# Kernel optimization log

Hardware: AMD Instinct MI355X
Metric: run time of the kernel (lower is better)

## Reference

```python
import jax, jax.numpy as jnp
import numpy as np

PAST = 12
FUTURE = 12


def setup_inputs() -> dict:
    key = jax.random.key(0)
    k1, k2, k3, k4, k5 = jax.random.split(key, 5)
    B, L, D = 64, 256, 512
    inp = jax.random.normal(k1, (B, L, D), dtype=jnp.float32)
    W_t = jax.random.normal(k2, (FUTURE, PAST), dtype=jnp.float32) / np.sqrt(PAST)
    b_t = jax.random.normal(k3, (FUTURE,), dtype=jnp.float32) * 0.01
    W_s = jax.random.normal(k4, (D, D), dtype=jnp.float32) / np.sqrt(D)
    b_s = jax.random.normal(k5, (D,), dtype=jnp.float32) * 0.01
    return {"inp": inp, "W_t": W_t, "b_t": b_t, "W_s": W_s, "b_s": b_s}


def reference(inp, W_t, b_t, W_s, b_s):
    # inp: [B, L, D]. Sliding windows of size PAST -> W = L - PAST windows.
    B, L, D = inp.shape
    W = L - PAST
    # gather windows: [B, W, PAST, D]
    idx = jnp.arange(W)[:, None] + jnp.arange(PAST)[None, :]  # [W, PAST]
    x_win = inp[:, idx, :]  # [B, W, PAST, D]
    # temporal Linear(PAST -> FUTURE) along window-time axis
    t = jnp.einsum('bwpd,fp->bwfd', x_win, W_t) + b_t[None, None, :, None]
    # spatial Linear(D -> D) along last axis
    out = jnp.einsum('bwfd,ed->bwfe', t, W_s) + b_s
    return out  # [B, W, FUTURE, D]
```

## Files before the change

kernel.cpp:

```cpp
#include <hip/hip_runtime.h>

#define PAST 12
#define FUTURE 12
#define NB 64
#define NL 256
#define ND 512
#define NW 244

typedef unsigned short ushort_t;
typedef __attribute__((ext_vector_type(8))) short short8;
typedef __attribute__((ext_vector_type(4))) float floatx4;

__device__ inline unsigned int f2bf(float x) {
    unsigned int u = __float_as_uint(x);
    return (u + 0x7fffu + ((u >> 16) & 1u)) >> 16;
}

__global__ __launch_bounds__(256) void convert_inp(
    const float* __restrict__ in, ushort_t* __restrict__ out)
{
    const int i = (blockIdx.x * 256 + threadIdx.x) * 8;
    const float4 v0 = *(const float4*)(in + i);
    const float4 v1 = *(const float4*)(in + i + 4);
    uint4 o;
    o.x = f2bf(v0.x) | (f2bf(v0.y) << 16);
    o.y = f2bf(v0.z) | (f2bf(v0.w) << 16);
    o.z = f2bf(v1.x) | (f2bf(v1.y) << 16);
    o.w = f2bf(v1.z) | (f2bf(v1.w) << 16);
    *(uint4*)(out + i) = o;
}

__global__ __launch_bounds__(256) void prep_ws(
    const float* __restrict__ Ws, ushort_t* __restrict__ Wsb, float* __restrict__ S)
{
    const int row = blockIdx.x;
    const int t = threadIdx.x;
    const float2 v = *(const float2*)(Ws + (size_t)row * ND + t * 2);
    *(unsigned int*)(Wsb + (size_t)row * ND + t * 2) = f2bf(v.x) | (f2bf(v.y) << 16);
    float s = v.x + v.y;
#pragma unroll
    for (int o = 32; o > 0; o >>= 1) s += __shfl_down(s, o);
    __shared__ float red[4];
    if ((t & 63) == 0) red[t >> 6] = s;
    __syncthreads();
    if (t == 0) S[row] = red[0] + red[1] + red[2] + red[3];
}

#define BM 128
#define BN 128
#define BK 32

__global__ __launch_bounds__(256) void gemm_spatial(
    const ushort_t* __restrict__ A,
    const ushort_t* __restrict__ Bm,
    ushort_t* __restrict__ Y)
{
    __shared__ ushort_t As[BM * BK];
    __shared__ ushort_t Bs[BN * BK];

    const int tid  = threadIdx.x;
    const int wave = tid >> 6;
    const int lane = tid & 63;
    const int m0 = blockIdx.y * BM;
    const int n0 = blockIdx.x * BN;
    const int wm = (wave >> 1) * 64;
    const int wn = (wave & 1) * 64;

    floatx4 acc[4][4] = {};

    const int row_a = tid >> 2;
    const int ch_a  = (tid & 3) * 8;

    for (int k0 = 0; k0 < ND; k0 += BK) {
        __syncthreads();
#pragma unroll
        for (int r = 0; r < 2; ++r) {
            const ushort_t* ga = A + (size_t)(m0 + row_a + r * 64) * ND + k0 + ch_a;
            __builtin_amdgcn_global_load_lds(
                (const __attribute__((address_space(1))) unsigned int*)ga,
                (__attribute__((address_space(3))) unsigned int*)(As + (r * 256 + wave * 64) * 8),
                16, 0, 0);
        }
#pragma unroll
        for (int r = 0; r < 2; ++r) {
            const ushort_t* gb = Bm + (size_t)(n0 + row_a + r * 64) * ND + k0 + ch_a;
            __builtin_amdgcn_global_load_lds(
                (const __attribute__((address_space(1))) unsigned int*)gb,
                (__attribute__((address_space(3))) unsigned int*)(Bs + (r * 256 + wave * 64) * 8),
                16, 0, 0);
        }
        __syncthreads();

        const ushort_t* a_base = As + (wm + (lane & 15)) * BK + (lane >> 4) * 8;
        const ushort_t* b_base = Bs + (wn + (lane & 15)) * BK + (lane >> 4) * 8;
        short8 a[4], b[4];
#pragma unroll
        for (int t = 0; t < 4; ++t) {
            a[t] = *(const short8*)(a_base + t * 16 * BK);
            b[t] = *(const short8*)(b_base + t * 16 * BK);
        }
#pragma unroll
        for (int i = 0; i < 4; ++i)
#pragma unroll
            for (int j = 0; j < 4; ++j)
                acc[i][j] = __builtin_amdgcn_mfma_f32_16x16x32_bf16(a[i], b[j], acc[i][j], 0, 0, 0);
    }

#pragma unroll
    for (int i = 0; i < 4; ++i) {
        const int m_base = m0 + wm + i * 16 + (lane >> 4) * 4;
#pragma unroll
        for (int j = 0; j < 4; ++j) {
            const int n = n0 + wn + j * 16 + (lane & 15);
#pragma unroll
            for (int r = 0; r < 4; ++r) {
                Y[(size_t)(m_base + r) * ND + n] = (ushort_t)f2bf(acc[i][j][r]);
            }
        }
    }
}

#define WTILE 8

__global__ __launch_bounds__(256) void temporal_kernel(
    const ushort_t* __restrict__ Y,
    const float*    __restrict__ Wt,
    const float*    __restrict__ bt,
    const float*    __restrict__ bs,
    const float*    __restrict__ S,
    float*          __restrict__ Out)
{
    const int tid = threadIdx.x;
    const int b  = blockIdx.y;
    const int w0 = blockIdx.x * WTILE + (tid >> 7) * 4;
    const int eq = (tid & 127) * 4;

    const float4 Sv  = *(const float4*)(S + eq);
    const float4 bsv = *(const float4*)(bs + eq);

    float win[PAST + 3][4];
    const ushort_t* ybase = Y + ((size_t)(b * NL + w0)) * ND + eq;
#pragma unroll
    for (int i = 0; i < PAST + 3; ++i) {
        if (w0 + i < NL) {
            const uint2 v = *(const uint2*)(ybase + (size_t)i * ND);
            win[i][0] = __uint_as_float(v.x << 16);
            win[i][1] = __uint_as_float(v.x & 0xffff0000u);
            win[i][2] = __uint_as_float(v.y << 16);
            win[i][3] = __uint_as_float(v.y & 0xffff0000u);
        } else {
            win[i][0] = win[i][1] = win[i][2] = win[i][3] = 0.f;
        }
    }

#pragma unroll
    for (int w = 0; w < 4; ++w) {
        if (w0 + w < NW) {
            float* orow = Out + ((size_t)(b * NW + (w0 + w)) * FUTURE) * ND + eq;
#pragma unroll
            for (int f = 0; f < FUTURE; ++f) {
                const float btf = bt[f];
                float a0 = fmaf(btf, Sv.x, bsv.x);
                float a1 = fmaf(btf, Sv.y, bsv.y);
                float a2 = fmaf(btf, Sv.z, bsv.z);
                float a3 = fmaf(btf, Sv.w, bsv.w);
#pragma unroll
                for (int p = 0; p < PAST; ++p) {
                    const float c = Wt[f * PAST + p];
                    a0 = fmaf(c, win[w + p][0], a0);
                    a1 = fmaf(c, win[w + p][1], a1);
                    a2 = fmaf(c, win[w + p][2], a2);
                    a3 = fmaf(c, win[w + p][3], a3);
                }
                *(float4*)(orow + (size_t)f * ND) = make_float4(a0, a1, a2, a3);
            }
        }
    }
}

extern "C" void kernel_launch(void* const* d_in, const int* in_sizes, int n_in,
                              void* d_out, int out_size, void* d_ws, size_t ws_size,
                              hipStream_t stream) {
    const float* inp = (const float*)d_in[0];
    const float* Wt  = (const float*)d_in[1];
    const float* bt  = (const float*)d_in[2];
    const float* Ws  = (const float*)d_in[3];
    const float* bs  = (const float*)d_in[4];
    float* out = (float*)d_out;

    const size_t n_inp = (size_t)NB * NL * ND;
    ushort_t* Y     = (ushort_t*)d_ws;
    ushort_t* inp_b = (ushort_t*)((char*)d_ws + n_inp * 2);
    ushort_t* Ws_b  = (ushort_t*)((char*)d_ws + n_inp * 4);
    float*    S     = (float*)((char*)d_ws + n_inp * 4 + (size_t)ND * ND * 2);

    convert_inp<<<dim3(n_inp / 8 / 256), dim3(256), 0, stream>>>(inp, inp_b);
    prep_ws<<<dim3(ND), dim3(256), 0, stream>>>(Ws, Ws_b, S);
    gemm_spatial<<<dim3(ND / BN, (NB * NL) / BM), dim3(256), 0, stream>>>(inp_b, Ws_b, Y);
    temporal_kernel<<<dim3((NW + WTILE - 1) / WTILE, NB), dim3(256), 0, stream>>>(Y, Wt, bt, bs, S, out);
}
```

Baseline: 427.2 us.

## Fuse input conversion, spatial GEMM and temporal projection into one kernel

Merges the fp32-to-bf16 conversion, the spatial GEMM and the temporal sliding-window kernel into a single kernel. Each block computes a 160-row (128 windows plus halo) by 128-column GEMM tile from fp32 input, converting to bf16 on the fly with double-buffered LDS, then keeps the bf16 result in LDS and applies the temporal projection directly. This removes the global round trips for the bf16 input copy and the intermediate Y tensor, and drops two launches. In exchange, halo rows are recomputed (160 rows computed for 128 windows), the grid is smaller (512 blocks), and the epilogue loops serially over 16 windows per thread group.

```diff
diff --git a/kernel.cpp b/kernel.cpp
--- a/kernel.cpp
+++ b/kernel.cpp
@@ -7,6 +7,10 @@
 #define ND 512
 #define NW 244
 
+#define LROWS 160
+#define BN2 128
+#define BK2 32
+
 typedef unsigned short ushort_t;
 typedef __attribute__((ext_vector_type(8))) short short8;
 typedef __attribute__((ext_vector_type(4))) float floatx4;
@@ -14,20 +18,6 @@
 __device__ inline unsigned int f2bf(float x) {
     unsigned int u = __float_as_uint(x);
     return (u + 0x7fffu + ((u >> 16) & 1u)) >> 16;
-}
-
-__global__ __launch_bounds__(256) void convert_inp(
-    const float* __restrict__ in, ushort_t* __restrict__ out)
-{
-    const int i = (blockIdx.x * 256 + threadIdx.x) * 8;
-    const float4 v0 = *(const float4*)(in + i);
-    const float4 v1 = *(const float4*)(in + i + 4);
-    uint4 o;
-    o.x = f2bf(v0.x) | (f2bf(v0.y) << 16);
-    o.y = f2bf(v0.z) | (f2bf(v0.w) << 16);
-    o.z = f2bf(v1.x) | (f2bf(v1.y) << 16);
-    o.w = f2bf(v1.z) | (f2bf(v1.w) << 16);
-    *(uint4*)(out + i) = o;
 }
 
 __global__ __launch_bounds__(256) void prep_ws(
@@ -46,134 +36,151 @@
     if (t == 0) S[row] = red[0] + red[1] + red[2] + red[3];
 }
 
-#define BM 128
-#define BN 128
-#define BK 32
-
-__global__ __launch_bounds__(256) void gemm_spatial(
-    const ushort_t* __restrict__ A,
+
+#define STAGE_A_LOAD(k0) do { \
+    _Pragma("unroll") \
+    for (int c = 0; c < 5; ++c) av[c] = *(const float4*)(aptr[c] + (k0)); \
+} while (0)
+
+#define STAGE_A_WRITE(dst) do { \
+    _Pragma("unroll") \
+    for (int c = 0; c < 5; ++c) { \
+        uint2 o; \
+        o.x = f2bf(av[c].x) | (f2bf(av[c].y) << 16); \
+        o.y = f2bf(av[c].z) | (f2bf(av[c].w) << 16); \
+        *(uint2*)((dst) + awoff + c * 1024) = o; \
+    } \
+} while (0)
+
+#define STAGE_B(k0, dst) do { \
+    _Pragma("unroll") \
+    for (int r = 0; r < 2; ++r) { \
+        const ushort_t* gb = Bm + (size_t)(n0 + (tid >> 2) + r * 64) * ND + (k0) + (tid & 3) * 8; \
+        __builtin_amdgcn_global_load_lds( \
+            (const __attribute__((address_space(1))) unsigned int*)gb, \
+            (__attribute__((address_space(3))) unsigned int*)((dst) + r * 2048 + tid * 8), \
+            16, 0, 0); \
+    } \
+} while (0)
+
+#define GEMM_STEP(cura, curb) do { \
+    const ushort_t* a_base = (cura) + (wm + (lane & 15)) * BK2 + (lane >> 4) * 8; \
+    const ushort_t* b_base = (curb) + (wn + (lane & 15)) * BK2 + (lane >> 4) * 8; \
+    short8 af[5], bq[4]; \
+    _Pragma("unroll") \
+    for (int mt = 0; mt < 5; ++mt) af[mt] = *(const short8*)(a_base + mt * 16 * BK2); \
+    _Pragma("unroll") \
+    for (int nt = 0; nt < 4; ++nt) bq[nt] = *(const short8*)(b_base + nt * 16 * BK2); \
+    _Pragma("unroll") \
+    for (int mt = 0; mt < 5; ++mt) \
+    _Pragma("unroll") \
+    for (int nt = 0; nt < 4; ++nt) \
+        acc[mt][nt] = __builtin_amdgcn_mfma_f32_16x16x32_bf16(af[mt], bq[nt], acc[mt][nt], 0, 0, 0); \
+} while (0)
+
+#define FULL_STEP(k, cura, curb, nxta, nxtb) do { \
+    if ((k) < 15) { STAGE_A_LOAD(((k) + 1) * BK2); STAGE_B(((k) + 1) * BK2, nxtb); } \
+    GEMM_STEP(cura, curb); \
+    if ((k) < 15) STAGE_A_WRITE(nxta); \
+    __syncthreads(); \
+} while (0)
+
+__global__ __launch_bounds__(256) void fused(
+    const float* __restrict__ A,
     const ushort_t* __restrict__ Bm,
-    ushort_t* __restrict__ Y)
+    const float* __restrict__ Wt,
+    const float* __restrict__ bt,
+    const float* __restrict__ bs,
+    const float* __restrict__ S,
+    float* __restrict__ Out)
 {
-    __shared__ ushort_t As[BM * BK];
-    __shared__ ushort_t Bs[BN * BK];
+    __shared__ __align__(16) ushort_t lds[LROWS * BN2];
 
     const int tid  = threadIdx.x;
+    const int lane = tid & 63;
     const int wave = tid >> 6;
-    const int lane = tid & 63;
-    const int m0 = blockIdx.y * BM;
-    const int n0 = blockIdx.x * BN;
-    const int wm = (wave >> 1) * 64;
+    const int wm = (wave >> 1) * 80;
     const int wn = (wave & 1) * 64;
-
-    floatx4 acc[4][4] = {};
-
-    const int row_a = tid >> 2;
-    const int ch_a  = (tid & 3) * 8;
-
-    for (int k0 = 0; k0 < ND; k0 += BK) {
-        __syncthreads();
-#pragma unroll
-        for (int r = 0; r < 2; ++r) {
-            const ushort_t* ga = A + (size_t)(m0 + row_a + r * 64) * ND + k0 + ch_a;
-            __builtin_amdgcn_global_load_lds(
-                (const __attribute__((address_space(1))) unsigned int*)ga,
-                (__attribute__((address_space(3))) unsigned int*)(As + (r * 256 + wave * 64) * 8),
-                16, 0, 0);
+    const int n0 = blockIdx.x * BN2;
+    const int b  = blockIdx.y >> 1;
+    const int lt = blockIdx.y & 1;
+
+    ushort_t* const As0 = lds;
+    ushort_t* const As1 = lds + LROWS * BK2;
+    ushort_t* const Bs0 = lds + 2 * LROWS * BK2;
+    ushort_t* const Bs1 = lds + 2 * LROWS * BK2 + BN2 * BK2;
+
+    const float* aptr[5];
+#pragma unroll
+    for (int c = 0; c < 5; ++c) {
+        const int i = c * 256 + tid;
+        const int row = i >> 3;
+        const int rcl = (lt * 128 + row < NL) ? (lt * 128 + row) : (NL - 1);
+        aptr[c] = A + ((size_t)b * NL + rcl) * ND + (i & 7) * 4;
+    }
+    const int awoff = tid * 4;
+
+    float4 av[5];
+    floatx4 acc[5][4] = {};
+
+    STAGE_A_LOAD(0);
+    STAGE_B(0, Bs0);
+    STAGE_A_WRITE(As0);
+    __syncthreads();
+
+    for (int k = 0; k < 16; k += 2) {
+        FULL_STEP(k,     As0, Bs0, As1, Bs1);
+        FULL_STEP(k + 1, As1, Bs1, As0, Bs0);
+    }
+
+#pragma unroll
+    for (int mt = 0; mt < 5; ++mt) {
+        const int r0 = wm + mt * 16 + (lane >> 4) * 4;
+#pragma unroll
+        for (int nt = 0; nt < 4; ++nt) {
+            const int cc = wn + nt * 16 + (lane & 15);
+#pragma unroll
+            for (int r = 0; r < 4; ++r)
+                lds[(r0 + r) * BN2 + cc] = (ushort_t)f2bf(acc[mt][nt][r]);
         }
-#pragma unroll
-        for (int r = 0; r < 2; ++r) {
-            const ushort_t* gb = Bm + (size_t)(n0 + row_a + r * 64) * ND + k0 + ch_a;
-            __builtin_amdgcn_global_load_lds(
-                (const __attribute__((address_space(1))) unsigned int*)gb,
-                (__attribute__((address_space(3))) unsigned int*)(Bs + (r * 256 + wave * 64) * 8),
-                16, 0, 0);
+    }
+    __syncthreads();
+
+    const int eq4  = (tid & 31) * 4;
+    const int wg   = tid >> 5;
+    const int wlim = lt ? (NW - 128) : 128;
+    const int wbeg = wg * 16;
+    const int wend = (wbeg + 16 < wlim) ? (wbeg + 16) : wlim;
+    const float4 Sv  = *(const float4*)(S + n0 + eq4);
+    const float4 bsv = *(const float4*)(bs + n0 + eq4);
+
+    for (int wl = wbeg; wl < wend; ++wl) {
+        float win[PAST][4];
+#pragma unroll
+        for (int p = 0; p < PAST; ++p) {
+            const uint2 v = *(const uint2*)(lds + (wl + p) * BN2 + eq4);
+            win[p][0] = __uint_as_float(v.x << 16);
+            win[p][1] = __uint_as_float(v.x & 0xffff0000u);
+            win[p][2] = __uint_as_float(v.y << 16);
+            win[p][3] = __uint_as_float(v.y & 0xffff0000u);
         }
-        __syncthreads();
-
-        const ushort_t* a_base = As + (wm + (lane & 15)) * BK + (lane >> 4) * 8;
-        const ushort_t* b_base = Bs + (wn + (lane & 15)) * BK + (lane >> 4) * 8;
-        short8 a[4], b[4];
-#pragma unroll
-        for (int t = 0; t < 4; ++t) {
-            a[t] = *(const short8*)(a_base + t * 16 * BK);
-            b[t] = *(const short8*)(b_base + t * 16 * BK);
-        }
-#pragma unroll
-        for (int i = 0; i < 4; ++i)
-#pragma unroll
-            for (int j = 0; j < 4; ++j)
-                acc[i][j] = __builtin_amdgcn_mfma_f32_16x16x32_bf16(a[i], b[j], acc[i][j], 0, 0, 0);
-    }
-
-#pragma unroll
-    for (int i = 0; i < 4; ++i) {
-        const int m_base = m0 + wm + i * 16 + (lane >> 4) * 4;
-#pragma unroll
-        for (int j = 0; j < 4; ++j) {
-            const int n = n0 + wn + j * 16 + (lane & 15);
-#pragma unroll
-            for (int r = 0; r < 4; ++r) {
-                Y[(size_t)(m_base + r) * ND + n] = (ushort_t)f2bf(acc[i][j][r]);
+        float* orow = Out + ((size_t)(b * NW + lt * 128 + wl) * FUTURE) * ND + n0 + eq4;
+#pragma unroll
+        for (int f = 0; f < FUTURE; ++f) {
+            const float btf = bt[f];
+            float a0 = fmaf(btf, Sv.x, bsv.x);
+            float a1 = fmaf(btf, Sv.y, bsv.y);
+            float a2 = fmaf(btf, Sv.z, bsv.z);
+            float a3 = fmaf(btf, Sv.w, bsv.w);
+#pragma unroll
+            for (int p = 0; p < PAST; ++p) {
+                const float c = Wt[f * PAST + p];
+                a0 = fmaf(c, win[p][0], a0);
+                a1 = fmaf(c, win[p][1], a1);
+                a2 = fmaf(c, win[p][2], a2);
+                a3 = fmaf(c, win[p][3], a3);
             }
-        }
-    }
-}
-
-#define WTILE 8
-
-__global__ __launch_bounds__(256) void temporal_kernel(
-    const ushort_t* __restrict__ Y,
-    const float*    __restrict__ Wt,
-    const float*    __restrict__ bt,
-    const float*    __restrict__ bs,
-    const float*    __restrict__ S,
-    float*          __restrict__ Out)
-{
-    const int tid = threadIdx.x;
-    const int b  = blockIdx.y;
-    const int w0 = blockIdx.x * WTILE + (tid >> 7) * 4;
-    const int eq = (tid & 127) * 4;
-
-    const float4 Sv  = *(const float4*)(S + eq);
-    const float4 bsv = *(const float4*)(bs + eq);
-
-    float win[PAST + 3][4];
-    const ushort_t* ybase = Y + ((size_t)(b * NL + w0)) * ND + eq;
-#pragma unroll
-    for (int i = 0; i < PAST + 3; ++i) {
-        if (w0 + i < NL) {
-            const uint2 v = *(const uint2*)(ybase + (size_t)i * ND);
-            win[i][0] = __uint_as_float(v.x << 16);
-            win[i][1] = __uint_as_float(v.x & 0xffff0000u);
-            win[i][2] = __uint_as_float(v.y << 16);
-            win[i][3] = __uint_as_float(v.y & 0xffff0000u);
-        } else {
-            win[i][0] = win[i][1] = win[i][2] = win[i][3] = 0.f;
-        }
-    }
-
-#pragma unroll
-    for (int w = 0; w < 4; ++w) {
-        if (w0 + w < NW) {
-            float* orow = Out + ((size_t)(b * NW + (w0 + w)) * FUTURE) * ND + eq;
-#pragma unroll
-            for (int f = 0; f < FUTURE; ++f) {
-                const float btf = bt[f];
-                float a0 = fmaf(btf, Sv.x, bsv.x);
-                float a1 = fmaf(btf, Sv.y, bsv.y);
-                float a2 = fmaf(btf, Sv.z, bsv.z);
-                float a3 = fmaf(btf, Sv.w, bsv.w);
-#pragma unroll
-                for (int p = 0; p < PAST; ++p) {
-                    const float c = Wt[f * PAST + p];
-                    a0 = fmaf(c, win[w + p][0], a0);
-                    a1 = fmaf(c, win[w + p][1], a1);
-                    a2 = fmaf(c, win[w + p][2], a2);
-                    a3 = fmaf(c, win[w + p][3], a3);
-                }
-                *(float4*)(orow + (size_t)f * ND) = make_float4(a0, a1, a2, a3);
-            }
+            *(float4*)(orow + (size_t)f * ND) = make_float4(a0, a1, a2, a3);
         }
     }
 }
@@ -188,14 +195,9 @@
     const float* bs  = (const float*)d_in[4];
     float* out = (float*)d_out;
 
-    const size_t n_inp = (size_t)NB * NL * ND;
-    ushort_t* Y     = (ushort_t*)d_ws;
-    ushort_t* inp_b = (ushort_t*)((char*)d_ws + n_inp * 2);
-    ushort_t* Ws_b  = (ushort_t*)((char*)d_ws + n_inp * 4);
-    float*    S     = (float*)((char*)d_ws + n_inp * 4 + (size_t)ND * ND * 2);
-
-    convert_inp<<<dim3(n_inp / 8 / 256), dim3(256), 0, stream>>>(inp, inp_b);
+    ushort_t* Ws_b = (ushort_t*)d_ws;
+    float*    S    = (float*)((char*)d_ws + (size_t)ND * ND * sizeof(ushort_t));
+
     prep_ws<<<dim3(ND), dim3(256), 0, stream>>>(Ws, Ws_b, S);
-    gemm_spatial<<<dim3(ND / BN, (NB * NL) / BM), dim3(256), 0, stream>>>(inp_b, Ws_b, Y);
-    temporal_kernel<<<dim3((NW + WTILE - 1) / WTILE, NB), dim3(256), 0, stream>>>(Y, Wt, bt, bs, S, out);
-}
+    fused<<<dim3(ND / BN2, NB * 2), dim3(256), 0, stream>>>(inp, Ws_b, Wt, bt, bs, S, out);
+}
```

Result: slower. 501.1 us (+17.3%).

## Fuse fp32-to-bf16 input conversion into GEMM with double-buffered LDS pipeline

Applied to the files above, without the earlier changes.

Drops the separate convert_inp kernel. The GEMM now reads fp32 input directly, converts it to bf16 in registers and writes it into LDS. LDS is double-buffered, so the next tile's global loads are issued before the current tile's MFMAs. This removes a full extra read and write of the input and one kernel launch. In exchange, each K-step does more global traffic per GEMM block, because fp32 A is read once per N-tile (four times in total), and it uses more LDS and registers.

```diff
diff --git a/kernel.cpp b/kernel.cpp
--- a/kernel.cpp
+++ b/kernel.cpp
@@ -14,20 +14,6 @@
 __device__ inline unsigned int f2bf(float x) {
     unsigned int u = __float_as_uint(x);
     return (u + 0x7fffu + ((u >> 16) & 1u)) >> 16;
-}
-
-__global__ __launch_bounds__(256) void convert_inp(
-    const float* __restrict__ in, ushort_t* __restrict__ out)
-{
-    const int i = (blockIdx.x * 256 + threadIdx.x) * 8;
-    const float4 v0 = *(const float4*)(in + i);
-    const float4 v1 = *(const float4*)(in + i + 4);
-    uint4 o;
-    o.x = f2bf(v0.x) | (f2bf(v0.y) << 16);
-    o.y = f2bf(v0.z) | (f2bf(v0.w) << 16);
-    o.z = f2bf(v1.x) | (f2bf(v1.y) << 16);
-    o.w = f2bf(v1.z) | (f2bf(v1.w) << 16);
-    *(uint4*)(out + i) = o;
 }
 
 __global__ __launch_bounds__(256) void prep_ws(
@@ -50,13 +36,64 @@
 #define BN 128
 #define BK 32
 
+#define STAGE_A_LOAD(k0) do { \
+    _Pragma("unroll") \
+    for (int c = 0; c < 4; ++c) av[c] = *(const float4*)(aptr[c] + (k0)); \
+} while (0)
+
+#define STAGE_A_WRITE(dst) do { \
+    _Pragma("unroll") \
+    for (int c = 0; c < 4; ++c) { \
+        uint2 o; \
+        o.x = f2bf(av[c].x) | (f2bf(av[c].y) << 16); \
+        o.y = f2bf(av[c].z) | (f2bf(av[c].w) << 16); \
+        *(uint2*)((dst) + tid * 4 + c * 1024) = o; \
+    } \
+} while (0)
+
+#define STAGE_B(k0, dst) do { \
+    _Pragma("unroll") \
+    for (int r = 0; r < 2; ++r) { \
+        const ushort_t* gb = Bm + (size_t)(n0 + (tid >> 2) + r * 64) * ND + (k0) + (tid & 3) * 8; \
+        __builtin_amdgcn_global_load_lds( \
+            (const __attribute__((address_space(1))) unsigned int*)gb, \
+            (__attribute__((address_space(3))) unsigned int*)((dst) + r * 2048 + tid * 8), \
+            16, 0, 0); \
+    } \
+} while (0)
+
+#define GEMM_STEP(cura, curb) do { \
+    const ushort_t* a_base = (cura) + (wm + (lane & 15)) * BK + (lane >> 4) * 8; \
+    const ushort_t* b_base = (curb) + (wn + (lane & 15)) * BK + (lane >> 4) * 8; \
+    short8 af[4], bq[4]; \
+    _Pragma("unroll") \
+    for (int t = 0; t < 4; ++t) { \
+        af[t] = *(const short8*)(a_base + t * 16 * BK); \
+        bq[t] = *(const short8*)(b_base + t * 16 * BK); \
+    } \
+    _Pragma("unroll") \
+    for (int i = 0; i < 4; ++i) \
+    _Pragma("unroll") \
+    for (int j = 0; j < 4; ++j) \
+        acc[i][j] = __builtin_amdgcn_mfma_f32_16x16x32_bf16(af[i], bq[j], acc[i][j], 0, 0, 0); \
+} while (0)
+
+#define FULL_STEP(k, cura, curb, nxta, nxtb) do { \
+    if ((k) < 15) { STAGE_A_LOAD(((k) + 1) * BK); STAGE_B(((k) + 1) * BK, nxtb); } \
+    GEMM_STEP(cura, curb); \
+    if ((k) < 15) STAGE_A_WRITE(nxta); \
+    __syncthreads(); \
+} while (0)
+
 __global__ __launch_bounds__(256) void gemm_spatial(
-    const ushort_t* __restrict__ A,
+    const float* __restrict__ A,
     const ushort_t* __restrict__ Bm,
     ushort_t* __restrict__ Y)
 {
-    __shared__ ushort_t As[BM * BK];
-    __shared__ ushort_t Bs[BN * BK];
+    __shared__ __align__(16) ushort_t As0[BM * BK];
+    __shared__ __align__(16) ushort_t As1[BM * BK];
+    __shared__ __align__(16) ushort_t Bs0[BN * BK];
+    __shared__ __align__(16) ushort_t Bs1[BN * BK];
 
     const int tid  = threadIdx.x;
     const int wave = tid >> 6;
@@ -68,42 +105,23 @@
 
     floatx4 acc[4][4] = {};
 
-    const int row_a = tid >> 2;
-    const int ch_a  = (tid & 3) * 8;
-
-    for (int k0 = 0; k0 < ND; k0 += BK) {
-        __syncthreads();
-#pragma unroll
-        for (int r = 0; r < 2; ++r) {
-            const ushort_t* ga = A + (size_t)(m0 + row_a + r * 64) * ND + k0 + ch_a;
-            __builtin_amdgcn_global_load_lds(
-                (const __attribute__((address_space(1))) unsigned int*)ga,
-                (__attribute__((address_space(3))) unsigned int*)(As + (r * 256 + wave * 64) * 8),
-                16, 0, 0);
-        }
-#pragma unroll
-        for (int r = 0; r < 2; ++r) {
-            const ushort_t* gb = Bm + (size_t)(n0 + row_a + r * 64) * ND + k0 + ch_a;
-            __builtin_amdgcn_global_load_lds(
-                (const __attribute__((address_space(1))) unsigned int*)gb,
-                (__attribute__((address_space(3))) unsigned int*)(Bs + (r * 256 + wave * 64) * 8),
-                16, 0, 0);
-        }
-        __syncthreads();
-
-        const ushort_t* a_base = As + (wm + (lane & 15)) * BK + (lane >> 4) * 8;
-        const ushort_t* b_base = Bs + (wn + (lane & 15)) * BK + (lane >> 4) * 8;
-        short8 a[4], b[4];
-#pragma unroll
-        for (int t = 0; t < 4; ++t) {
-            a[t] = *(const short8*)(a_base + t * 16 * BK);
-            b[t] = *(const short8*)(b_base + t * 16 * BK);
-        }
-#pragma unroll
-        for (int i = 0; i < 4; ++i)
-#pragma unroll
-            for (int j = 0; j < 4; ++j)
-                acc[i][j] = __builtin_amdgcn_mfma_f32_16x16x32_bf16(a[i], b[j], acc[i][j], 0, 0, 0);
+    const float* aptr[4];
+#pragma unroll
+    for (int c = 0; c < 4; ++c) {
+        const int i = c * 256 + tid;
+        aptr[c] = A + (size_t)(m0 + (i >> 3)) * ND + (i & 7) * 4;
+    }
+
+    float4 av[4];
+
+    STAGE_A_LOAD(0);
+    STAGE_B(0, Bs0);
+    STAGE_A_WRITE(As0);
+    __syncthreads();
+
+    for (int k = 0; k < 16; k += 2) {
+        FULL_STEP(k,     As0, Bs0, As1, Bs1);
+        FULL_STEP(k + 1, As1, Bs1, As0, Bs0);
     }
 
 #pragma unroll
@@ -189,13 +207,11 @@
     float* out = (float*)d_out;
 
     const size_t n_inp = (size_t)NB * NL * ND;
-    ushort_t* Y     = (ushort_t*)d_ws;
-    ushort_t* inp_b = (ushort_t*)((char*)d_ws + n_inp * 2);
-    ushort_t* Ws_b  = (ushort_t*)((char*)d_ws + n_inp * 4);
-    float*    S     = (float*)((char*)d_ws + n_inp * 4 + (size_t)ND * ND * 2);
-
-    convert_inp<<<dim3(n_inp / 8 / 256), dim3(256), 0, stream>>>(inp, inp_b);
+    ushort_t* Y    = (ushort_t*)d_ws;
+    ushort_t* Ws_b = (ushort_t*)((char*)d_ws + n_inp * 2);
+    float*    S    = (float*)((char*)d_ws + n_inp * 2 + (size_t)ND * ND * 2);
+
     prep_ws<<<dim3(ND), dim3(256), 0, stream>>>(Ws, Ws_b, S);
-    gemm_spatial<<<dim3(ND / BN, (NB * NL) / BM), dim3(256), 0, stream>>>(inp_b, Ws_b, Y);
+    gemm_spatial<<<dim3(ND / BN, (NB * NL) / BM), dim3(256), 0, stream>>>(inp, Ws_b, Y);
     temporal_kernel<<<dim3((NW + WTILE - 1) / WTILE, NB), dim3(256), 0, stream>>>(Y, Wt, bt, bs, S, out);
 }
```

New measurement: 437.6 us. 2.4% more time.
